# Kernel tuning notes

Measured on AMD Instinct MI355X. Metric: run time of the kernel, lower is better.

The kernel has to match this reference:

```python
import jax, jax.numpy as jnp
import numpy as np

N_HEADS = 16
DIM_HEAD = 64
ROPE_THETA = 10000.0


def _rope_tables(seq_len, dim_head, dtype):
    # [N, dim_head//2] angle tables, llama-style interleaved-pair rotation
    inv_freq = 1.0 / (ROPE_THETA ** (jnp.arange(0, dim_head, 2, dtype=jnp.float32) / dim_head))
    t = jnp.arange(seq_len, dtype=jnp.float32)
    freqs = jnp.outer(t, inv_freq)  # [N, D/2]
    return jnp.cos(freqs).astype(dtype), jnp.sin(freqs).astype(dtype)


def _apply_rope(x, cos, sin):
    # x: [B, H, N, D]; rotate interleaved pairs (x[2i], x[2i+1])
    xr = x[..., 0::2]
    xi = x[..., 1::2]
    cos = cos[None, None, :, :]
    sin = sin[None, None, :, :]
    out_r = xr * cos - xi * sin
    out_i = xr * sin + xi * cos
    return jnp.stack([out_r, out_i], axis=-1).reshape(x.shape)


def _l2norm(x, eps=1e-12):
    return x / jnp.maximum(jnp.linalg.norm(x, axis=-1, keepdims=True), eps)


def setup_inputs() -> dict:
    key = jax.random.key(0)
    ks = jax.random.split(key, 5)
    B, N, dim = 1, 4096, N_HEADS * DIM_HEAD
    q = jax.random.normal(ks[0], (B, N, dim), dtype=jnp.float32)
    k = jax.random.normal(ks[1], (B, N, dim), dtype=jnp.float32)
    v = jax.random.normal(ks[2], (B, N, dim), dtype=jnp.float32)
    qk_scale = jnp.full((1, 1, 1, DIM_HEAD), 10.0, dtype=jnp.float32)
    w_out = jax.random.normal(ks[3], (dim, dim), dtype=jnp.float32) * (dim ** -0.5)
    b_out = jnp.zeros((dim,), dtype=jnp.float32)
    return {"q": q, "k": k, "v": v, "qk_scale": qk_scale, "w_out": w_out, "b_out": b_out}


def reference(q, k, v, qk_scale, w_out, b_out):
    B, N, dim = q.shape
    H, D = N_HEADS, DIM_HEAD
    scale = D ** -0.5
    # [B, N, dim] -> [B, H, N, D]
    q = q.reshape(B, N, H, D).transpose(0, 2, 1, 3)
    k = k.reshape(B, N, H, D).transpose(0, 2, 1, 3)
    v = v.reshape(B, N, H, D).transpose(0, 2, 1, 3)
    # RoPE
    cos, sin = _rope_tables(N, D, q.dtype)
    q = _apply_rope(q, cos, sin)
    k = _apply_rope(k, cos, sin)
    # QK-norm: L2-normalize then learned scale
    q = _l2norm(q) * qk_scale
    k = _l2norm(k) * qk_scale
    # explicit attention (non-flash)
    scores = jnp.einsum('bhid,bhjd->bhij', q, k) * scale
    probs = jax.nn.softmax(scores, axis=-1)
    out = jnp.einsum('bhij,bhjd->bhid', probs, v)
    out = out.transpose(0, 2, 1, 3).reshape(B, N, dim)
    # Linear: y = x W^T + b
    return out @ w_out.T + b_out
```

## Files before the change

kernel.cpp:

```cpp
#include <hip/hip_runtime.h>
#include <hip/hip_bf16.h>

#define N_CTX 4096
#define NH    16
#define DH    64
#define DIM   1024

typedef __attribute__((ext_vector_type(8))) short bf16x8;
typedef __attribute__((ext_vector_type(4))) float f32x4;

__device__ __forceinline__ ushort f2bf(float f) {
    union { float f; unsigned u; } x; x.f = f;
    unsigned r = (x.u + 0x7FFFu + ((x.u >> 16) & 1u)) >> 16;
    return (ushort)r;
}
__device__ __forceinline__ ushort f2bf_fast(float f) {
    union { float f; unsigned u; } x; x.f = f;
    return (ushort)((x.u + 0x8000u) >> 16);
}

__global__ __launch_bounds__(256) void prep_kernel(
    const float* __restrict__ x, const float* __restrict__ qk_scale,
    ushort* __restrict__ xb)
{
    const int lane = threadIdx.x & 63;
    const int wave = threadIdx.x >> 6;
    const int row  = blockIdx.x * 4 + wave;
    const int n = row >> 4;
    const int h = row & 15;

    float val = x[(size_t)n * DIM + h * DH + lane];
    float other = __shfl_xor(val, 1, 64);

    const int i = lane >> 1;
    float inv_freq = 1.0f / powf(10000.0f, (float)i * (1.0f / 32.0f));
    float ang = (float)n * inv_freq;
    float s, c;
    sincosf(ang, &s, &c);

    float r = (lane & 1) ? fmaf(other, s, val * c)
                         : fmaf(val, c, -(other * s));

    float ss = r * r;
    #pragma unroll
    for (int off = 32; off > 0; off >>= 1)
        ss += __shfl_xor(ss, off, 64);
    float invn = 1.0f / fmaxf(sqrtf(ss), 1e-12f);
    float scl  = qk_scale[lane];

    xb[((size_t)h * N_CTX + n) * DH + lane] = f2bf(r * invn * scl);
}

__global__ __launch_bounds__(256) void vtrans_kernel(
    const float* __restrict__ v, ushort* __restrict__ vt)
{
    __shared__ ushort L[64][68];
    const int kt = blockIdx.x, h = blockIdx.y, t = threadIdx.x;

    for (int e = t; e < 4096; e += 256) {
        int key = e >> 6, d = e & 63;
        float f = v[(size_t)(kt * 64 + key) * DIM + h * DH + d];
        L[d][key] = f2bf(f);
    }
    __syncthreads();
    for (int e = t; e < 4096; e += 256) {
        int d = e >> 6, key = e & 63;
        vt[((size_t)h * DH + d) * N_CTX + kt * 64 + key] = L[d][key];
    }
}

__global__ __launch_bounds__(256) void wconv_kernel(
    const float* __restrict__ w, ushort* __restrict__ wb)
{
    int i = (blockIdx.x * 256 + threadIdx.x) * 4;
    float4 f = *(const float4*)&w[i];
    ushort4 u;
    u.x = f2bf(f.x); u.y = f2bf(f.y); u.z = f2bf(f.z); u.w = f2bf(f.w);
    *(ushort4*)&wb[i] = u;
}

#define SC 0.18033688011112042f
#define SB (-18.033688011112042f)

__global__ __launch_bounds__(512) void attn_kernel(
    const ushort* __restrict__ qb, const ushort* __restrict__ kb,
    const ushort* __restrict__ vt, ushort* __restrict__ attn_out)
{
    __shared__ ushort Ks[64][72];
    __shared__ ushort Vt[64][72];
    __shared__ ushort Ps[128][72];
    __shared__ float  Ls[4][128];

    const int h     = blockIdx.y;
    const int qbase = blockIdx.x * 128;
    const int t      = threadIdx.x;
    const int w      = t >> 6;
    const int lane   = t & 63;
    const int l15    = lane & 15;
    const int quad   = lane >> 4;
    const int kslice = (w & 3) * 16;
    const int qhalf  = (w >> 2) * 64;

    bf16x8 qf[4][2];
    #pragma unroll
    for (int nt = 0; nt < 4; nt++)
        #pragma unroll
        for (int ks = 0; ks < 2; ks++)
            qf[nt][ks] = *(const bf16x8*)&qb[((size_t)h * N_CTX + qbase + qhalf + nt * 16 + l15) * DH
                                             + ks * 32 + quad * 8];

    float l_part[4];
    f32x4 o_acc[4];
    #pragma unroll
    for (int nt = 0; nt < 4; nt++) l_part[nt] = 0.0f;
    #pragma unroll
    for (int dt = 0; dt < 4; dt++) o_acc[dt] = (f32x4){0.f, 0.f, 0.f, 0.f};

    for (int kt = 0; kt < N_CTX / 64; kt++) {
        __syncthreads();
        {
            int r = t >> 3, c8 = t & 7;
            *(bf16x8*)&Ks[r][c8 * 8] =
                *(const bf16x8*)&kb[((size_t)h * N_CTX + kt * 64 + r) * DH + c8 * 8];
            *(bf16x8*)&Vt[r][c8 * 8] =
                *(const bf16x8*)&vt[((size_t)h * DH + r) * N_CTX + kt * 64 + c8 * 8];
        }
        __syncthreads();

        bf16x8 kf0 = *(const bf16x8*)&Ks[kslice + l15][quad * 8];
        bf16x8 kf1 = *(const bf16x8*)&Ks[kslice + l15][32 + quad * 8];

        #pragma unroll
        for (int nt = 0; nt < 4; nt++) {
            f32x4 s = (f32x4){0.f, 0.f, 0.f, 0.f};
            s = __builtin_amdgcn_mfma_f32_16x16x32_bf16(kf0, qf[nt][0], s, 0, 0, 0);
            s = __builtin_amdgcn_mfma_f32_16x16x32_bf16(kf1, qf[nt][1], s, 0, 0, 0);

            float p0 = exp2f(fmaf(s.x, SC, SB));
            float p1 = exp2f(fmaf(s.y, SC, SB));
            float p2 = exp2f(fmaf(s.z, SC, SB));
            float p3 = exp2f(fmaf(s.w, SC, SB));
            l_part[nt] += (p0 + p1) + (p2 + p3);
            ushort4 pk;
            pk.x = f2bf_fast(p0); pk.y = f2bf_fast(p1);
            pk.z = f2bf_fast(p2); pk.w = f2bf_fast(p3);
            *(ushort4*)&Ps[qhalf + nt * 16 + l15][kslice + quad * 4] = pk;
        }
        __syncthreads();

        #pragma unroll
        for (int ks = 0; ks < 2; ks++) {
            bf16x8 pf = *(const bf16x8*)&Ps[w * 16 + l15][ks * 32 + quad * 8];
            #pragma unroll
            for (int dt = 0; dt < 4; dt++) {
                bf16x8 vf = *(const bf16x8*)&Vt[dt * 16 + l15][ks * 32 + quad * 8];
                o_acc[dt] = __builtin_amdgcn_mfma_f32_16x16x32_bf16(vf, pf, o_acc[dt], 0, 0, 0);
            }
        }
    }

    #pragma unroll
    for (int nt = 0; nt < 4; nt++) {
        float v = l_part[nt];
        v += __shfl_xor(v, 16, 64);
        v += __shfl_xor(v, 32, 64);
        l_part[nt] = v;
    }
    if (quad == 0) {
        #pragma unroll
        for (int nt = 0; nt < 4; nt++)
            Ls[w & 3][qhalf + nt * 16 + l15] = l_part[nt];
    }
    __syncthreads();

    {
        int q = w * 16 + l15;
        float linv = 1.0f / ((Ls[0][q] + Ls[1][q]) + (Ls[2][q] + Ls[3][q]));
        #pragma unroll
        for (int dt = 0; dt < 4; dt++) {
            f32x4 o = o_acc[dt];
            ushort4 ov;
            ov.x = f2bf_fast(o.x * linv); ov.y = f2bf_fast(o.y * linv);
            ov.z = f2bf_fast(o.z * linv); ov.w = f2bf_fast(o.w * linv);
            *(ushort4*)&attn_out[(size_t)(qbase + q) * DIM + h * DH + dt * 16 + quad * 4] = ov;
        }
    }
}

__global__ __launch_bounds__(256) void proj_kernel(
    const ushort* __restrict__ A, const ushort* __restrict__ W,
    const float* __restrict__ bias, float* __restrict__ out)
{
    __shared__ ushort As[128][72];
    __shared__ ushort Ws[64][72];

    const int nbase = blockIdx.x * 128;
    const int obase = blockIdx.y * 64;
    const int t    = threadIdx.x;
    const int w    = t >> 6;
    const int lane = t & 63;
    const int l15  = lane & 15;
    const int quad = lane >> 4;
    const int rw   = (w >> 1) * 64;
    const int cw   = (w & 1) * 32;

    f32x4 acc[4][2];
    #pragma unroll
    for (int mt = 0; mt < 4; mt++)
        #pragma unroll
        for (int nt = 0; nt < 2; nt++)
            acc[mt][nt] = (f32x4){0.f, 0.f, 0.f, 0.f};

    for (int kt = 0; kt < DIM / 64; kt++) {
        const int kb = kt * 64;
        __syncthreads();
        #pragma unroll
        for (int i = 0; i < 4; i++) {
            int c = t + i * 256, r = c >> 3, c8 = c & 7;
            *(bf16x8*)&As[r][c8 * 8] =
                *(const bf16x8*)&A[(size_t)(nbase + r) * DIM + kb + c8 * 8];
        }
        #pragma unroll
        for (int i = 0; i < 2; i++) {
            int c = t + i * 256, r = c >> 3, c8 = c & 7;
            *(bf16x8*)&Ws[r][c8 * 8] =
                *(const bf16x8*)&W[(size_t)(obase + r) * DIM + kb + c8 * 8];
        }
        __syncthreads();

        bf16x8 af[4][2], bfr[2][2];
        #pragma unroll
        for (int mt = 0; mt < 4; mt++)
            #pragma unroll
            for (int kh = 0; kh < 2; kh++)
                af[mt][kh] = *(const bf16x8*)&As[rw + mt * 16 + l15][kh * 32 + quad * 8];
        #pragma unroll
        for (int nt = 0; nt < 2; nt++)
            #pragma unroll
            for (int kh = 0; kh < 2; kh++)
                bfr[nt][kh] = *(const bf16x8*)&Ws[cw + nt * 16 + l15][kh * 32 + quad * 8];

        #pragma unroll
        for (int mt = 0; mt < 4; mt++)
            #pragma unroll
            for (int nt = 0; nt < 2; nt++) {
                acc[mt][nt] = __builtin_amdgcn_mfma_f32_16x16x32_bf16(af[mt][0], bfr[nt][0], acc[mt][nt], 0, 0, 0);
                acc[mt][nt] = __builtin_amdgcn_mfma_f32_16x16x32_bf16(af[mt][1], bfr[nt][1], acc[mt][nt], 0, 0, 0);
            }
    }

    #pragma unroll
    for (int nt = 0; nt < 2; nt++) {
        int o = obase + cw + nt * 16 + l15;
        float bb = bias[o];
        #pragma unroll
        for (int mt = 0; mt < 4; mt++) {
            int nrow = nbase + rw + mt * 16 + quad * 4;
            out[(size_t)(nrow + 0) * DIM + o] = acc[mt][nt].x + bb;
            out[(size_t)(nrow + 1) * DIM + o] = acc[mt][nt].y + bb;
            out[(size_t)(nrow + 2) * DIM + o] = acc[mt][nt].z + bb;
            out[(size_t)(nrow + 3) * DIM + o] = acc[mt][nt].w + bb;
        }
    }
}

extern "C" void kernel_launch(void* const* d_in, const int* in_sizes, int n_in,
                              void* d_out, int out_size, void* d_ws, size_t ws_size,
                              hipStream_t stream)
{
    const float* q        = (const float*)d_in[0];
    const float* k        = (const float*)d_in[1];
    const float* v        = (const float*)d_in[2];
    const float* qk_scale = (const float*)d_in[3];
    const float* w_out    = (const float*)d_in[4];
    const float* b_out    = (const float*)d_in[5];
    float* out = (float*)d_out;

    const size_t per = (size_t)NH * N_CTX * DH;
    ushort* qb    = (ushort*)d_ws;
    ushort* kb    = qb + per;
    ushort* vtg   = kb + per;
    ushort* attnb = vtg + per;
    ushort* wb    = attnb + per;

    prep_kernel<<<dim3(N_CTX * NH / 4), 256, 0, stream>>>(q, qk_scale, qb);
    prep_kernel<<<dim3(N_CTX * NH / 4), 256, 0, stream>>>(k, qk_scale, kb);
    vtrans_kernel<<<dim3(N_CTX / 64, NH), 256, 0, stream>>>(v, vtg);
    wconv_kernel<<<dim3(DIM * DIM / 1024), 256, 0, stream>>>(w_out, wb);
    attn_kernel<<<dim3(N_CTX / 128, NH), 512, 0, stream>>>(qb, kb, vtg, attnb);
    proj_kernel<<<dim3(N_CTX / 128, DIM / 64), 256, 0, stream>>>(attnb, wb, b_out, out);
}
```

Before: 291.0 us.

## Split attention over key halves with combine kernel, register prefetch and per-wave rows

The attention kernel now splits the key range in two across a third grid dimension. Each block writes unnormalised fp32 partial outputs and row sums, and a new combine kernel adds the two halves, normalises and converts to bf16. Each wave now owns 16 query rows across all 64 keys of a tile, so its P tile stays wave-private and the barrier between writing P and the PV MFMAs is dropped. K/V tiles are prefetched into registers one iteration ahead, and exp2 and bf16 packing use hardware intrinsics. This doubles the block count and shortens the per-block serial loop, at the cost of extra global traffic for the fp32 partial outputs and one more kernel launch.

```diff
diff --git a/kernel.cpp b/kernel.cpp
--- a/kernel.cpp
+++ b/kernel.cpp
@@ -5,6 +5,8 @@
 #define NH    16
 #define DH    64
 #define DIM   1024
+#define NSPLIT 2
+#define KT_PER_SPLIT (N_CTX / 64 / NSPLIT)
 
 typedef __attribute__((ext_vector_type(8))) short bf16x8;
 typedef __attribute__((ext_vector_type(4))) float f32x4;
@@ -14,9 +16,32 @@
     unsigned r = (x.u + 0x7FFFu + ((x.u >> 16) & 1u)) >> 16;
     return (ushort)r;
 }
-__device__ __forceinline__ ushort f2bf_fast(float f) {
-    union { float f; unsigned u; } x; x.f = f;
-    return (ushort)((x.u + 0x8000u) >> 16);
+__device__ __forceinline__ unsigned fbits(float f) {
+    union { float f; unsigned u; } x; x.f = f; return x.u;
+}
+__device__ __forceinline__ unsigned pack_bf16(float lo, float hi) {
+    unsigned a = fbits(lo) + 0x8000u;
+    unsigned b = fbits(hi) + 0x8000u;
+#if defined(__has_builtin)
+#if __has_builtin(__builtin_amdgcn_perm)
+    return __builtin_amdgcn_perm(b, a, 0x07060302u);
+#else
+    return (a >> 16) | (b & 0xFFFF0000u);
+#endif
+#else
+    return (a >> 16) | (b & 0xFFFF0000u);
+#endif
+}
+__device__ __forceinline__ float fast_exp2(float x) {
+#if defined(__has_builtin)
+#if __has_builtin(__builtin_amdgcn_exp2f)
+    return __builtin_amdgcn_exp2f(x);
+#else
+    return exp2f(x);
+#endif
+#else
+    return exp2f(x);
+#endif
 }
 
 __global__ __launch_bounds__(256) void prep_kernel(
@@ -84,69 +109,67 @@
 
 __global__ __launch_bounds__(512) void attn_kernel(
     const ushort* __restrict__ qb, const ushort* __restrict__ kb,
-    const ushort* __restrict__ vt, ushort* __restrict__ attn_out)
+    const ushort* __restrict__ vt, float* __restrict__ opart,
+    float* __restrict__ lpart)
 {
     __shared__ ushort Ks[64][72];
     __shared__ ushort Vt[64][72];
     __shared__ ushort Ps[128][72];
-    __shared__ float  Ls[4][128];
 
     const int h     = blockIdx.y;
     const int qbase = blockIdx.x * 128;
-    const int t      = threadIdx.x;
-    const int w      = t >> 6;
-    const int lane   = t & 63;
-    const int l15    = lane & 15;
-    const int quad   = lane >> 4;
-    const int kslice = (w & 3) * 16;
-    const int qhalf  = (w >> 2) * 64;
-
-    bf16x8 qf[4][2];
-    #pragma unroll
-    for (int nt = 0; nt < 4; nt++)
-        #pragma unroll
-        for (int ks = 0; ks < 2; ks++)
-            qf[nt][ks] = *(const bf16x8*)&qb[((size_t)h * N_CTX + qbase + qhalf + nt * 16 + l15) * DH
-                                             + ks * 32 + quad * 8];
-
-    float l_part[4];
+    const int sp    = blockIdx.z;
+    const int kbase = sp * (N_CTX / NSPLIT);
+    const int t    = threadIdx.x;
+    const int w    = t >> 6;
+    const int lane = t & 63;
+    const int l15  = lane & 15;
+    const int quad = lane >> 4;
+
+    const size_t qrow = ((size_t)h * N_CTX + qbase + w * 16 + l15) * DH;
+    bf16x8 qf0 = *(const bf16x8*)&qb[qrow + quad * 8];
+    bf16x8 qf1 = *(const bf16x8*)&qb[qrow + 32 + quad * 8];
+
+    float l_part = 0.0f;
     f32x4 o_acc[4];
     #pragma unroll
-    for (int nt = 0; nt < 4; nt++) l_part[nt] = 0.0f;
-    #pragma unroll
     for (int dt = 0; dt < 4; dt++) o_acc[dt] = (f32x4){0.f, 0.f, 0.f, 0.f};
 
-    for (int kt = 0; kt < N_CTX / 64; kt++) {
+    const int sr = t >> 3;
+    const int sc = (t & 7) * 8;
+    const ushort* kptr = &kb[((size_t)h * N_CTX + kbase + sr) * DH + sc];
+    const ushort* vptr = &vt[((size_t)h * DH + sr) * N_CTX + kbase + sc];
+    bf16x8 kreg = *(const bf16x8*)kptr;
+    bf16x8 vreg = *(const bf16x8*)vptr;
+
+    for (int kt = 0; kt < KT_PER_SPLIT; kt++) {
         __syncthreads();
-        {
-            int r = t >> 3, c8 = t & 7;
-            *(bf16x8*)&Ks[r][c8 * 8] =
-                *(const bf16x8*)&kb[((size_t)h * N_CTX + kt * 64 + r) * DH + c8 * 8];
-            *(bf16x8*)&Vt[r][c8 * 8] =
-                *(const bf16x8*)&vt[((size_t)h * DH + r) * N_CTX + kt * 64 + c8 * 8];
-        }
+        *(bf16x8*)&Ks[sr][sc] = kreg;
+        *(bf16x8*)&Vt[sr][sc] = vreg;
         __syncthreads();
-
-        bf16x8 kf0 = *(const bf16x8*)&Ks[kslice + l15][quad * 8];
-        bf16x8 kf1 = *(const bf16x8*)&Ks[kslice + l15][32 + quad * 8];
-
-        #pragma unroll
-        for (int nt = 0; nt < 4; nt++) {
+        if (kt + 1 < KT_PER_SPLIT) {
+            kreg = *(const bf16x8*)(kptr + (size_t)(kt + 1) * 64 * DH);
+            vreg = *(const bf16x8*)(vptr + (size_t)(kt + 1) * 64);
+        }
+
+        #pragma unroll
+        for (int j = 0; j < 4; j++) {
+            bf16x8 kf0 = *(const bf16x8*)&Ks[j * 16 + l15][quad * 8];
+            bf16x8 kf1 = *(const bf16x8*)&Ks[j * 16 + l15][32 + quad * 8];
             f32x4 s = (f32x4){0.f, 0.f, 0.f, 0.f};
-            s = __builtin_amdgcn_mfma_f32_16x16x32_bf16(kf0, qf[nt][0], s, 0, 0, 0);
-            s = __builtin_amdgcn_mfma_f32_16x16x32_bf16(kf1, qf[nt][1], s, 0, 0, 0);
-
-            float p0 = exp2f(fmaf(s.x, SC, SB));
-            float p1 = exp2f(fmaf(s.y, SC, SB));
-            float p2 = exp2f(fmaf(s.z, SC, SB));
-            float p3 = exp2f(fmaf(s.w, SC, SB));
-            l_part[nt] += (p0 + p1) + (p2 + p3);
-            ushort4 pk;
-            pk.x = f2bf_fast(p0); pk.y = f2bf_fast(p1);
-            pk.z = f2bf_fast(p2); pk.w = f2bf_fast(p3);
-            *(ushort4*)&Ps[qhalf + nt * 16 + l15][kslice + quad * 4] = pk;
-        }
-        __syncthreads();
+            s = __builtin_amdgcn_mfma_f32_16x16x32_bf16(kf0, qf0, s, 0, 0, 0);
+            s = __builtin_amdgcn_mfma_f32_16x16x32_bf16(kf1, qf1, s, 0, 0, 0);
+
+            float p0 = fast_exp2(fmaf(s.x, SC, SB));
+            float p1 = fast_exp2(fmaf(s.y, SC, SB));
+            float p2 = fast_exp2(fmaf(s.z, SC, SB));
+            float p3 = fast_exp2(fmaf(s.w, SC, SB));
+            l_part += (p0 + p1) + (p2 + p3);
+            uint2 pk;
+            pk.x = pack_bf16(p0, p1);
+            pk.y = pack_bf16(p2, p3);
+            *(uint2*)&Ps[w * 16 + l15][j * 16 + quad * 4] = pk;
+        }
 
         #pragma unroll
         for (int ks = 0; ks < 2; ks++) {
@@ -159,32 +182,42 @@
         }
     }
 
-    #pragma unroll
-    for (int nt = 0; nt < 4; nt++) {
-        float v = l_part[nt];
-        v += __shfl_xor(v, 16, 64);
-        v += __shfl_xor(v, 32, 64);
-        l_part[nt] = v;
-    }
-    if (quad == 0) {
-        #pragma unroll
-        for (int nt = 0; nt < 4; nt++)
-            Ls[w & 3][qhalf + nt * 16 + l15] = l_part[nt];
-    }
-    __syncthreads();
-
-    {
-        int q = w * 16 + l15;
-        float linv = 1.0f / ((Ls[0][q] + Ls[1][q]) + (Ls[2][q] + Ls[3][q]));
-        #pragma unroll
-        for (int dt = 0; dt < 4; dt++) {
-            f32x4 o = o_acc[dt];
-            ushort4 ov;
-            ov.x = f2bf_fast(o.x * linv); ov.y = f2bf_fast(o.y * linv);
-            ov.z = f2bf_fast(o.z * linv); ov.w = f2bf_fast(o.w * linv);
-            *(ushort4*)&attn_out[(size_t)(qbase + q) * DIM + h * DH + dt * 16 + quad * 4] = ov;
-        }
-    }
+    l_part += __shfl_xor(l_part, 16, 64);
+    l_part += __shfl_xor(l_part, 32, 64);
+    if (quad == 0)
+        lpart[(size_t)sp * NH * N_CTX + (size_t)h * N_CTX + qbase + w * 16 + l15] = l_part;
+
+    #pragma unroll
+    for (int dt = 0; dt < 4; dt++) {
+        f32x4 o = o_acc[dt];
+        float4 ov; ov.x = o.x; ov.y = o.y; ov.z = o.z; ov.w = o.w;
+        *(float4*)&opart[((size_t)sp * N_CTX + qbase + w * 16 + l15) * DIM
+                         + h * DH + dt * 16 + quad * 4] = ov;
+    }
+}
+
+__global__ __launch_bounds__(256) void combine_kernel(
+    const float* __restrict__ opart, const float* __restrict__ lpart,
+    ushort* __restrict__ attnb)
+{
+    const int idx = blockIdx.x * 256 + threadIdx.x;
+    const int n   = idx >> 8;
+    const int rem = idx & 255;
+    const int h   = rem >> 4;
+    const size_t e = (size_t)n * DIM + h * DH + (rem & 15) * 4;
+
+    float4 o0 = *(const float4*)&opart[e];
+    float4 o1 = *(const float4*)&opart[(size_t)N_CTX * DIM + e];
+    float l0 = lpart[(size_t)h * N_CTX + n];
+    float l1 = lpart[(size_t)NH * N_CTX + (size_t)h * N_CTX + n];
+    float li = 1.0f / (l0 + l1);
+
+    ushort4 r;
+    r.x = f2bf((o0.x + o1.x) * li);
+    r.y = f2bf((o0.y + o1.y) * li);
+    r.z = f2bf((o0.z + o1.z) * li);
+    r.w = f2bf((o0.w + o1.w) * li);
+    *(ushort4*)&attnb[e] = r;
 }
 
 __global__ __launch_bounds__(256) void proj_kernel(
@@ -282,11 +315,14 @@
     ushort* vtg   = kb + per;
     ushort* attnb = vtg + per;
     ushort* wb    = attnb + per;
+    float*  opart = (float*)(wb + (size_t)DIM * DIM);
+    float*  lpart = opart + (size_t)NSPLIT * N_CTX * DIM;
 
     prep_kernel<<<dim3(N_CTX * NH / 4), 256, 0, stream>>>(q, qk_scale, qb);
     prep_kernel<<<dim3(N_CTX * NH / 4), 256, 0, stream>>>(k, qk_scale, kb);
     vtrans_kernel<<<dim3(N_CTX / 64, NH), 256, 0, stream>>>(v, vtg);
     wconv_kernel<<<dim3(DIM * DIM / 1024), 256, 0, stream>>>(w_out, wb);
-    attn_kernel<<<dim3(N_CTX / 128, NH), 512, 0, stream>>>(qb, kb, vtg, attnb);
+    attn_kernel<<<dim3(N_CTX / 128, NH, NSPLIT), 512, 0, stream>>>(qb, kb, vtg, opart, lpart);
+    combine_kernel<<<dim3(N_CTX * DIM / 4 / 256), 256, 0, stream>>>(opart, lpart, attnb);
     proj_kernel<<<dim3(N_CTX / 128, DIM / 64), 256, 0, stream>>>(attnb, wb, b_out, out);
 }
```

Result: faster. 274.5 us (-5.7%).
